# Performance work log

Measured on AMD Instinct MI355X. Metric: run time of the kernel, lower is better.

The kernel has to match this reference:

```python
import jax, jax.numpy as jnp
import numpy as np

B, T, D, U = 64, 4096, 256, 64

def setup_inputs() -> dict:
    key = jax.random.key(0)
    k1, k2, k3 = jax.random.split(key, 3)
    inputs = jax.random.normal(k1, (B, T, D), dtype=jnp.float32)
    # glorot_uniform init for W (D,U) and u (U,1); zeros bias
    limW = float(np.sqrt(6.0 / (D + U)))
    W = jax.random.uniform(k2, (D, U), minval=-limW, maxval=limW, dtype=jnp.float32)
    limu = float(np.sqrt(6.0 / (U + 1)))
    u = jax.random.uniform(k3, (U, 1), minval=-limu, maxval=limu, dtype=jnp.float32)
    b = jnp.zeros((U,), dtype=jnp.float32)
    return {"inputs": inputs, "W": W, "b": b, "u": u}

def reference(inputs, W, b, u):
    # score: [B,T,U] = tanh(inputs @ W + b)
    score = jnp.tanh(jnp.einsum('btd,du->btu', inputs, W) + b)
    # logits: [B,T,1]; softmax over time axis (axis=1)
    logits = jnp.einsum('btu,uo->bto', score, u)
    attention_weights = jax.nn.softmax(logits, axis=1)
    # weighted sum over time -> [B,D]
    context = jnp.sum(inputs * attention_weights, axis=1)
    return (context, attention_weights)
```

## Files before the change

kernel.cpp:

```cpp
#include <hip/hip_runtime.h>
#include <math.h>

#define B_ 64
#define T_ 4096
#define D_ 256
#define U_ 64
#define TM 64
#define ASTRIDE 264
#define TC 256

typedef float f32x4 __attribute__((ext_vector_type(4)));
typedef short bf16x8 __attribute__((ext_vector_type(8)));

__device__ __forceinline__ unsigned short f2bf_rne(float f) {
    unsigned u = __float_as_uint(f);
    unsigned r = u + 0x7fffu + ((u >> 16) & 1u);
    return (unsigned short)(r >> 16);
}
__device__ __forceinline__ float bfbits2f(unsigned short s) {
    return __uint_as_float(((unsigned)s) << 16);
}

__global__ __launch_bounds__(256) void wprep_kernel(
    const float* __restrict__ W, unsigned short* __restrict__ whi,
    unsigned short* __restrict__ wlo)
{
    int fi = blockIdx.x * 256 + threadIdx.x;
    int j    = fi & 7;
    int lane = (fi >> 3) & 63;
    int tile = fi >> 9;
    int nt = tile & 3, ks = tile >> 2;
    int k = ks * 32 + (lane >> 4) * 8 + j;
    int n = nt * 16 + (lane & 15);
    float w = W[k * U_ + n];
    unsigned short hi = f2bf_rne(w);
    unsigned short lo = f2bf_rne(w - bfbits2f(hi));
    whi[fi] = hi;
    wlo[fi] = lo;
}

__global__ __launch_bounds__(256) void logits_mfma(
    const float* __restrict__ x, const unsigned short* __restrict__ whi,
    const unsigned short* __restrict__ wlo, const float* __restrict__ bias,
    const float* __restrict__ uvec, float* __restrict__ logits)
{
    __shared__ unsigned short Ahi[TM * ASTRIDE];
    __shared__ unsigned short Alo[TM * ASTRIDE];

    int tid = threadIdx.x;
    const float4* xb = (const float4*)(x + (size_t)blockIdx.x * TM * D_);

#pragma unroll
    for (int i = 0; i < 16; ++i) {
        int f = tid + i * 256;
        int row = f >> 6, c4 = f & 63;
        float4 v = xb[f];
        unsigned short h0 = f2bf_rne(v.x), h1 = f2bf_rne(v.y),
                       h2 = f2bf_rne(v.z), h3 = f2bf_rne(v.w);
        unsigned short l0 = f2bf_rne(v.x - bfbits2f(h0)),
                       l1 = f2bf_rne(v.y - bfbits2f(h1)),
                       l2 = f2bf_rne(v.z - bfbits2f(h2)),
                       l3 = f2bf_rne(v.w - bfbits2f(h3));
        int base = row * ASTRIDE + c4 * 4;
        uint2 hp = { (unsigned)h0 | ((unsigned)h1 << 16),
                     (unsigned)h2 | ((unsigned)h3 << 16) };
        uint2 lp = { (unsigned)l0 | ((unsigned)l1 << 16),
                     (unsigned)l2 | ((unsigned)l3 << 16) };
        *(uint2*)(&Ahi[base]) = hp;
        *(uint2*)(&Alo[base]) = lp;
    }
    __syncthreads();

    int lane = tid & 63, wid = tid >> 6;
    int q = lane >> 4, r = lane & 15;

    f32x4 acc[4];
#pragma unroll
    for (int nt = 0; nt < 4; ++nt) acc[nt] = (f32x4){0.f, 0.f, 0.f, 0.f};

    const bf16x8* whiV = (const bf16x8*)whi;
    const bf16x8* wloV = (const bf16x8*)wlo;

#pragma unroll
    for (int ks = 0; ks < 8; ++ks) {
        int aoff = (wid * 16 + r) * ASTRIDE + ks * 32 + q * 8;
        bf16x8 ahi = *(const bf16x8*)(&Ahi[aoff]);
        bf16x8 alo = *(const bf16x8*)(&Alo[aoff]);
#pragma unroll
        for (int nt = 0; nt < 4; ++nt) {
            bf16x8 bhi = whiV[(ks * 4 + nt) * 64 + lane];
            bf16x8 blo = wloV[(ks * 4 + nt) * 64 + lane];
            acc[nt] = __builtin_amdgcn_mfma_f32_16x16x32_bf16(ahi, bhi, acc[nt], 0, 0, 0);
            acc[nt] = __builtin_amdgcn_mfma_f32_16x16x32_bf16(ahi, blo, acc[nt], 0, 0, 0);
            acc[nt] = __builtin_amdgcn_mfma_f32_16x16x32_bf16(alo, bhi, acc[nt], 0, 0, 0);
        }
    }

    float p0 = 0.f, p1 = 0.f, p2 = 0.f, p3 = 0.f;
#pragma unroll
    for (int nt = 0; nt < 4; ++nt) {
        int col = nt * 16 + r;
        float bv = bias[col], uv = uvec[col];
        float s0 = acc[nt][0] + bv, s1 = acc[nt][1] + bv,
              s2 = acc[nt][2] + bv, s3 = acc[nt][3] + bv;
        p0 = fmaf(1.f - 2.f / (__expf(2.f * s0) + 1.f), uv, p0);
        p1 = fmaf(1.f - 2.f / (__expf(2.f * s1) + 1.f), uv, p1);
        p2 = fmaf(1.f - 2.f / (__expf(2.f * s2) + 1.f), uv, p2);
        p3 = fmaf(1.f - 2.f / (__expf(2.f * s3) + 1.f), uv, p3);
    }
#pragma unroll
    for (int off = 1; off < 16; off <<= 1) {
        p0 += __shfl_xor(p0, off, 64);
        p1 += __shfl_xor(p1, off, 64);
        p2 += __shfl_xor(p2, off, 64);
        p3 += __shfl_xor(p3, off, 64);
    }
    if (r == 0) {
        float4 o = {p0, p1, p2, p3};
        *(float4*)(logits + (size_t)blockIdx.x * TM + wid * 16 + q * 4) = o;
    }
}

__global__ __launch_bounds__(256) void softmax_kernel(float* __restrict__ wts)
{
    int b = blockIdx.x;
    float* wp = wts + (size_t)b * T_;
    int tid = threadIdx.x;
    int wave = tid >> 6, lane = tid & 63;

    float vals[T_ / 256];
#pragma unroll
    for (int i = 0; i < T_ / 256; ++i) vals[i] = wp[tid + i * 256];

    float m = -INFINITY;
#pragma unroll
    for (int i = 0; i < T_ / 256; ++i) m = fmaxf(m, vals[i]);
#pragma unroll
    for (int off = 32; off >= 1; off >>= 1)
        m = fmaxf(m, __shfl_down(m, off, 64));

    __shared__ float smax[4], ssum[4];
    if (lane == 0) smax[wave] = m;
    __syncthreads();
    if (tid == 0)
        smax[0] = fmaxf(fmaxf(smax[0], smax[1]), fmaxf(smax[2], smax[3]));
    __syncthreads();
    m = smax[0];

    float s = 0.f;
#pragma unroll
    for (int i = 0; i < T_ / 256; ++i) {
        vals[i] = __expf(vals[i] - m);
        s += vals[i];
    }
#pragma unroll
    for (int off = 32; off >= 1; off >>= 1)
        s += __shfl_down(s, off, 64);
    if (lane == 0) ssum[wave] = s;
    __syncthreads();
    if (tid == 0) ssum[0] = ssum[0] + ssum[1] + ssum[2] + ssum[3];
    __syncthreads();

    float inv = 1.f / ssum[0];
#pragma unroll
    for (int i = 0; i < T_ / 256; ++i) wp[tid + i * 256] = vals[i] * inv;
}

__global__ __launch_bounds__(256) void context_kernel(
    const float* __restrict__ x, const float* __restrict__ wts,
    float* __restrict__ ctx)
{
    int b = blockIdx.y;
    int t0 = blockIdx.x * TC;
    int d = threadIdx.x;
    const float* xp = x + ((size_t)b * T_ + t0) * D_ + d;
    const float* wp = wts + (size_t)b * T_ + t0;

    float acc[8];
#pragma unroll
    for (int j = 0; j < 8; ++j) acc[j] = 0.f;

    for (int i = 0; i < TC; i += 8) {
        float w[8], xv[8];
#pragma unroll
        for (int j = 0; j < 8; ++j) w[j] = wp[i + j];
#pragma unroll
        for (int j = 0; j < 8; ++j) xv[j] = xp[(size_t)(i + j) * D_];
#pragma unroll
        for (int j = 0; j < 8; ++j) acc[j] = fmaf(w[j], xv[j], acc[j]);
    }
    float s = ((acc[0] + acc[1]) + (acc[2] + acc[3])) +
              ((acc[4] + acc[5]) + (acc[6] + acc[7]));
    atomicAdd(&ctx[b * D_ + d], s);
}

extern "C" void kernel_launch(void* const* d_in, const int* in_sizes, int n_in,
                              void* d_out, int out_size, void* d_ws, size_t ws_size,
                              hipStream_t stream) {
    const float* x    = (const float*)d_in[0];
    const float* W    = (const float*)d_in[1];
    const float* bias = (const float*)d_in[2];
    const float* uvec = (const float*)d_in[3];

    float* out = (float*)d_out;
    float* ctx = out;
    float* wts = out + B_ * D_;

    unsigned short* whi = (unsigned short*)d_ws;
    unsigned short* wlo = whi + D_ * U_;

    hipMemsetAsync(ctx, 0, B_ * D_ * sizeof(float), stream);

    wprep_kernel<<<D_ * U_ / 256, 256, 0, stream>>>(W, whi, wlo);
    logits_mfma<<<(B_ * T_) / TM, 256, 0, stream>>>(x, whi, wlo, bias, uvec, wts);
    softmax_kernel<<<B_, 256, 0, stream>>>(wts);
    context_kernel<<<dim3(T_ / TC, B_), 256, 0, stream>>>(x, wts, ctx);
}
```

Baseline: 458.0 us.

## Load A fragments directly from global and vectorize context reduction with float4

The logits kernel drops its shared-memory staging of the bf16 hi/lo split. Each lane now loads its 8 floats for every k-step straight from global memory and converts them in registers, which removes about 66KB of LDS and a barrier and so should raise occupancy. The cost is strided per-row global reads instead of fully coalesced ones. The context kernel switches to float4 loads, with four time-slices per block reduced through shared memory before the atomics, which cuts per-thread load count.

```diff
diff --git a/kernel.cpp b/kernel.cpp
--- a/kernel.cpp
+++ b/kernel.cpp
@@ -6,7 +6,6 @@
 #define D_ 256
 #define U_ 64
 #define TM 64
-#define ASTRIDE 264
 #define TC 256
 
 typedef float f32x4 __attribute__((ext_vector_type(4)));
@@ -44,36 +43,13 @@
     const unsigned short* __restrict__ wlo, const float* __restrict__ bias,
     const float* __restrict__ uvec, float* __restrict__ logits)
 {
-    __shared__ unsigned short Ahi[TM * ASTRIDE];
-    __shared__ unsigned short Alo[TM * ASTRIDE];
-
     int tid = threadIdx.x;
-    const float4* xb = (const float4*)(x + (size_t)blockIdx.x * TM * D_);
-
-#pragma unroll
-    for (int i = 0; i < 16; ++i) {
-        int f = tid + i * 256;
-        int row = f >> 6, c4 = f & 63;
-        float4 v = xb[f];
-        unsigned short h0 = f2bf_rne(v.x), h1 = f2bf_rne(v.y),
-                       h2 = f2bf_rne(v.z), h3 = f2bf_rne(v.w);
-        unsigned short l0 = f2bf_rne(v.x - bfbits2f(h0)),
-                       l1 = f2bf_rne(v.y - bfbits2f(h1)),
-                       l2 = f2bf_rne(v.z - bfbits2f(h2)),
-                       l3 = f2bf_rne(v.w - bfbits2f(h3));
-        int base = row * ASTRIDE + c4 * 4;
-        uint2 hp = { (unsigned)h0 | ((unsigned)h1 << 16),
-                     (unsigned)h2 | ((unsigned)h3 << 16) };
-        uint2 lp = { (unsigned)l0 | ((unsigned)l1 << 16),
-                     (unsigned)l2 | ((unsigned)l3 << 16) };
-        *(uint2*)(&Ahi[base]) = hp;
-        *(uint2*)(&Alo[base]) = lp;
-    }
-    __syncthreads();
-
     int lane = tid & 63, wid = tid >> 6;
     int q = lane >> 4, r = lane & 15;
 
+    size_t row = (size_t)blockIdx.x * TM + wid * 16 + r;
+    const float* xrow = x + row * D_;
+
     f32x4 acc[4];
 #pragma unroll
     for (int nt = 0; nt < 4; ++nt) acc[nt] = (f32x4){0.f, 0.f, 0.f, 0.f};
@@ -83,16 +59,24 @@
 
 #pragma unroll
     for (int ks = 0; ks < 8; ++ks) {
-        int aoff = (wid * 16 + r) * ASTRIDE + ks * 32 + q * 8;
-        bf16x8 ahi = *(const bf16x8*)(&Ahi[aoff]);
-        bf16x8 alo = *(const bf16x8*)(&Alo[aoff]);
+        int k0 = ks * 32 + q * 8;
+        float4 va = *(const float4*)(xrow + k0);
+        float4 vb = *(const float4*)(xrow + k0 + 4);
+        float f[8] = {va.x, va.y, va.z, va.w, vb.x, vb.y, vb.z, vb.w};
+        union { bf16x8 v; unsigned short s[8]; } ahi, alo;
+#pragma unroll
+        for (int j = 0; j < 8; ++j) {
+            unsigned short h = f2bf_rne(f[j]);
+            ahi.s[j] = h;
+            alo.s[j] = f2bf_rne(f[j] - bfbits2f(h));
+        }
 #pragma unroll
         for (int nt = 0; nt < 4; ++nt) {
             bf16x8 bhi = whiV[(ks * 4 + nt) * 64 + lane];
             bf16x8 blo = wloV[(ks * 4 + nt) * 64 + lane];
-            acc[nt] = __builtin_amdgcn_mfma_f32_16x16x32_bf16(ahi, bhi, acc[nt], 0, 0, 0);
-            acc[nt] = __builtin_amdgcn_mfma_f32_16x16x32_bf16(ahi, blo, acc[nt], 0, 0, 0);
-            acc[nt] = __builtin_amdgcn_mfma_f32_16x16x32_bf16(alo, bhi, acc[nt], 0, 0, 0);
+            acc[nt] = __builtin_amdgcn_mfma_f32_16x16x32_bf16(ahi.v, bhi, acc[nt], 0, 0, 0);
+            acc[nt] = __builtin_amdgcn_mfma_f32_16x16x32_bf16(ahi.v, blo, acc[nt], 0, 0, 0);
+            acc[nt] = __builtin_amdgcn_mfma_f32_16x16x32_bf16(alo.v, bhi, acc[nt], 0, 0, 0);
         }
     }
 
@@ -172,26 +156,55 @@
 {
     int b = blockIdx.y;
     int t0 = blockIdx.x * TC;
-    int d = threadIdx.x;
-    const float* xp = x + ((size_t)b * T_ + t0) * D_ + d;
-    const float* wp = wts + (size_t)b * T_ + t0;
-
-    float acc[8];
-#pragma unroll
-    for (int j = 0; j < 8; ++j) acc[j] = 0.f;
-
-    for (int i = 0; i < TC; i += 8) {
-        float w[8], xv[8];
-#pragma unroll
-        for (int j = 0; j < 8; ++j) w[j] = wp[i + j];
-#pragma unroll
-        for (int j = 0; j < 8; ++j) xv[j] = xp[(size_t)(i + j) * D_];
-#pragma unroll
-        for (int j = 0; j < 8; ++j) acc[j] = fmaf(w[j], xv[j], acc[j]);
-    }
-    float s = ((acc[0] + acc[1]) + (acc[2] + acc[3])) +
-              ((acc[4] + acc[5]) + (acc[6] + acc[7]));
-    atomicAdd(&ctx[b * D_ + d], s);
+    int tid = threadIdx.x;
+    int d4 = tid & 63;
+    int ts = tid >> 6;
+
+    const float4* xp = (const float4*)(x + ((size_t)b * T_ + t0) * D_) + d4;
+    const float* wp = wts + (size_t)b * T_ + t0 + ts;
+
+    float4 a0 = {0,0,0,0}, a1 = a0, a2 = a0, a3 = a0;
+#pragma unroll 4
+    for (int j = 0; j < TC / 4; j += 4) {
+        float w0 = wp[4 * (j + 0)];
+        float w1 = wp[4 * (j + 1)];
+        float w2 = wp[4 * (j + 2)];
+        float w3 = wp[4 * (j + 3)];
+        float4 x0 = xp[(size_t)(ts + 4 * (j + 0)) * 64];
+        float4 x1 = xp[(size_t)(ts + 4 * (j + 1)) * 64];
+        float4 x2 = xp[(size_t)(ts + 4 * (j + 2)) * 64];
+        float4 x3 = xp[(size_t)(ts + 4 * (j + 3)) * 64];
+        a0.x = fmaf(w0, x0.x, a0.x); a0.y = fmaf(w0, x0.y, a0.y);
+        a0.z = fmaf(w0, x0.z, a0.z); a0.w = fmaf(w0, x0.w, a0.w);
+        a1.x = fmaf(w1, x1.x, a1.x); a1.y = fmaf(w1, x1.y, a1.y);
+        a1.z = fmaf(w1, x1.z, a1.z); a1.w = fmaf(w1, x1.w, a1.w);
+        a2.x = fmaf(w2, x2.x, a2.x); a2.y = fmaf(w2, x2.y, a2.y);
+        a2.z = fmaf(w2, x2.z, a2.z); a2.w = fmaf(w2, x2.w, a2.w);
+        a3.x = fmaf(w3, x3.x, a3.x); a3.y = fmaf(w3, x3.y, a3.y);
+        a3.z = fmaf(w3, x3.z, a3.z); a3.w = fmaf(w3, x3.w, a3.w);
+    }
+    float4 s;
+    s.x = (a0.x + a1.x) + (a2.x + a3.x);
+    s.y = (a0.y + a1.y) + (a2.y + a3.y);
+    s.z = (a0.z + a1.z) + (a2.z + a3.z);
+    s.w = (a0.w + a1.w) + (a2.w + a3.w);
+
+    __shared__ float4 red[4][64];
+    red[ts][d4] = s;
+    __syncthreads();
+    if (ts == 0) {
+        float4 r0 = red[0][d4], r1 = red[1][d4], r2 = red[2][d4], r3 = red[3][d4];
+        float4 t;
+        t.x = (r0.x + r1.x) + (r2.x + r3.x);
+        t.y = (r0.y + r1.y) + (r2.y + r3.y);
+        t.z = (r0.z + r1.z) + (r2.z + r3.z);
+        t.w = (r0.w + r1.w) + (r2.w + r3.w);
+        float* c = ctx + b * D_ + d4 * 4;
+        atomicAdd(c + 0, t.x);
+        atomicAdd(c + 1, t.y);
+        atomicAdd(c + 2, t.z);
+        atomicAdd(c + 3, t.w);
+    }
 }
 
 extern "C" void kernel_launch(void* const* d_in, const int* in_sizes, int n_in,
```

Measured after the change: 424.3 us. -7.4%, faster.

## Fuse softmax into the logits kernel and stream a bf16 copy of x to context

Applied to the files above, without the earlier changes.

The logits kernel now keeps the split-bf16 W in LDS and reads x straight from global memory, with no A-tile staging. It writes exp(logit) with no max subtraction, plus per-block partial sums of the normaliser, so the separate softmax kernel is removed. It also writes a bf16 copy of x, and the context kernel reads that half-size copy to form the weighted sum, normalising by the summed partials. The aim is to cut one launch and the fp32 re-read of x, at the cost of extra writes, lower precision in context, and overflow risk if logits are ever large.

```diff
diff --git a/kernel.cpp b/kernel.cpp
--- a/kernel.cpp
+++ b/kernel.cpp
@@ -5,8 +5,7 @@
 #define T_ 4096
 #define D_ 256
 #define U_ 64
-#define TM 64
-#define ASTRIDE 264
+#define TM 128
 #define TC 256
 
 typedef float f32x4 __attribute__((ext_vector_type(4)));
@@ -42,156 +41,162 @@
 __global__ __launch_bounds__(256) void logits_mfma(
     const float* __restrict__ x, const unsigned short* __restrict__ whi,
     const unsigned short* __restrict__ wlo, const float* __restrict__ bias,
-    const float* __restrict__ uvec, float* __restrict__ logits)
+    const float* __restrict__ uvec, float* __restrict__ wts,
+    unsigned short* __restrict__ xbf, float* __restrict__ Zp)
 {
-    __shared__ unsigned short Ahi[TM * ASTRIDE];
-    __shared__ unsigned short Alo[TM * ASTRIDE];
+    __shared__ unsigned short Bh[16384];
+    __shared__ unsigned short Bl[16384];
+    __shared__ float zred[4];
 
     int tid = threadIdx.x;
-    const float4* xb = (const float4*)(x + (size_t)blockIdx.x * TM * D_);
-
-#pragma unroll
-    for (int i = 0; i < 16; ++i) {
-        int f = tid + i * 256;
-        int row = f >> 6, c4 = f & 63;
-        float4 v = xb[f];
-        unsigned short h0 = f2bf_rne(v.x), h1 = f2bf_rne(v.y),
-                       h2 = f2bf_rne(v.z), h3 = f2bf_rne(v.w);
-        unsigned short l0 = f2bf_rne(v.x - bfbits2f(h0)),
-                       l1 = f2bf_rne(v.y - bfbits2f(h1)),
-                       l2 = f2bf_rne(v.z - bfbits2f(h2)),
-                       l3 = f2bf_rne(v.w - bfbits2f(h3));
-        int base = row * ASTRIDE + c4 * 4;
-        uint2 hp = { (unsigned)h0 | ((unsigned)h1 << 16),
-                     (unsigned)h2 | ((unsigned)h3 << 16) };
-        uint2 lp = { (unsigned)l0 | ((unsigned)l1 << 16),
-                     (unsigned)l2 | ((unsigned)l3 << 16) };
-        *(uint2*)(&Ahi[base]) = hp;
-        *(uint2*)(&Alo[base]) = lp;
+    {
+        const uint4* sh = (const uint4*)whi;
+        const uint4* sl = (const uint4*)wlo;
+        uint4* dh = (uint4*)Bh;
+        uint4* dl = (uint4*)Bl;
+#pragma unroll
+        for (int i = 0; i < 8; ++i) {
+            dh[tid + i * 256] = sh[tid + i * 256];
+            dl[tid + i * 256] = sl[tid + i * 256];
+        }
     }
     __syncthreads();
 
     int lane = tid & 63, wid = tid >> 6;
     int q = lane >> 4, r = lane & 15;
-
-    f32x4 acc[4];
-#pragma unroll
-    for (int nt = 0; nt < 4; ++nt) acc[nt] = (f32x4){0.f, 0.f, 0.f, 0.f};
-
-    const bf16x8* whiV = (const bf16x8*)whi;
-    const bf16x8* wloV = (const bf16x8*)wlo;
-
-#pragma unroll
+    size_t R0 = (size_t)blockIdx.x * TM;
+    size_t row0 = R0 + wid * 16 + r;
+    size_t row1 = row0 + 64;
+    const float* x0 = x + row0 * D_;
+    const float* x1 = x + row1 * D_;
+    unsigned short* xo0 = xbf + row0 * D_;
+    unsigned short* xo1 = xbf + row1 * D_;
+
+    f32x4 acc0[4], acc1[4];
+#pragma unroll
+    for (int nt = 0; nt < 4; ++nt) {
+        acc0[nt] = (f32x4){0.f, 0.f, 0.f, 0.f};
+        acc1[nt] = (f32x4){0.f, 0.f, 0.f, 0.f};
+    }
+
+    const bf16x8* BhV = (const bf16x8*)Bh;
+    const bf16x8* BlV = (const bf16x8*)Bl;
+
+#pragma unroll 4
     for (int ks = 0; ks < 8; ++ks) {
-        int aoff = (wid * 16 + r) * ASTRIDE + ks * 32 + q * 8;
-        bf16x8 ahi = *(const bf16x8*)(&Ahi[aoff]);
-        bf16x8 alo = *(const bf16x8*)(&Alo[aoff]);
+        int k0 = ks * 32 + q * 8;
+        float4 va0 = *(const float4*)(x0 + k0);
+        float4 vb0 = *(const float4*)(x0 + k0 + 4);
+        float4 va1 = *(const float4*)(x1 + k0);
+        float4 vb1 = *(const float4*)(x1 + k0 + 4);
+        float f0[8] = {va0.x, va0.y, va0.z, va0.w, vb0.x, vb0.y, vb0.z, vb0.w};
+        float f1[8] = {va1.x, va1.y, va1.z, va1.w, vb1.x, vb1.y, vb1.z, vb1.w};
+        union { bf16x8 v; unsigned short s[8]; uint4 u; } h0, l0, h1, l1;
+#pragma unroll
+        for (int j = 0; j < 8; ++j) {
+            unsigned short a = f2bf_rne(f0[j]);
+            h0.s[j] = a;
+            l0.s[j] = f2bf_rne(f0[j] - bfbits2f(a));
+            unsigned short c = f2bf_rne(f1[j]);
+            h1.s[j] = c;
+            l1.s[j] = f2bf_rne(f1[j] - bfbits2f(c));
+        }
+        *(uint4*)(xo0 + k0) = h0.u;
+        *(uint4*)(xo1 + k0) = h1.u;
 #pragma unroll
         for (int nt = 0; nt < 4; ++nt) {
-            bf16x8 bhi = whiV[(ks * 4 + nt) * 64 + lane];
-            bf16x8 blo = wloV[(ks * 4 + nt) * 64 + lane];
-            acc[nt] = __builtin_amdgcn_mfma_f32_16x16x32_bf16(ahi, bhi, acc[nt], 0, 0, 0);
-            acc[nt] = __builtin_amdgcn_mfma_f32_16x16x32_bf16(ahi, blo, acc[nt], 0, 0, 0);
-            acc[nt] = __builtin_amdgcn_mfma_f32_16x16x32_bf16(alo, bhi, acc[nt], 0, 0, 0);
-        }
-    }
-
-    float p0 = 0.f, p1 = 0.f, p2 = 0.f, p3 = 0.f;
-#pragma unroll
-    for (int nt = 0; nt < 4; ++nt) {
-        int col = nt * 16 + r;
-        float bv = bias[col], uv = uvec[col];
-        float s0 = acc[nt][0] + bv, s1 = acc[nt][1] + bv,
-              s2 = acc[nt][2] + bv, s3 = acc[nt][3] + bv;
-        p0 = fmaf(1.f - 2.f / (__expf(2.f * s0) + 1.f), uv, p0);
-        p1 = fmaf(1.f - 2.f / (__expf(2.f * s1) + 1.f), uv, p1);
-        p2 = fmaf(1.f - 2.f / (__expf(2.f * s2) + 1.f), uv, p2);
-        p3 = fmaf(1.f - 2.f / (__expf(2.f * s3) + 1.f), uv, p3);
-    }
-#pragma unroll
-    for (int off = 1; off < 16; off <<= 1) {
-        p0 += __shfl_xor(p0, off, 64);
-        p1 += __shfl_xor(p1, off, 64);
-        p2 += __shfl_xor(p2, off, 64);
-        p3 += __shfl_xor(p3, off, 64);
-    }
-    if (r == 0) {
-        float4 o = {p0, p1, p2, p3};
-        *(float4*)(logits + (size_t)blockIdx.x * TM + wid * 16 + q * 4) = o;
-    }
-}
-
-__global__ __launch_bounds__(256) void softmax_kernel(float* __restrict__ wts)
-{
-    int b = blockIdx.x;
-    float* wp = wts + (size_t)b * T_;
-    int tid = threadIdx.x;
-    int wave = tid >> 6, lane = tid & 63;
-
-    float vals[T_ / 256];
-#pragma unroll
-    for (int i = 0; i < T_ / 256; ++i) vals[i] = wp[tid + i * 256];
-
-    float m = -INFINITY;
-#pragma unroll
-    for (int i = 0; i < T_ / 256; ++i) m = fmaxf(m, vals[i]);
-#pragma unroll
-    for (int off = 32; off >= 1; off >>= 1)
-        m = fmaxf(m, __shfl_down(m, off, 64));
-
-    __shared__ float smax[4], ssum[4];
-    if (lane == 0) smax[wave] = m;
-    __syncthreads();
-    if (tid == 0)
-        smax[0] = fmaxf(fmaxf(smax[0], smax[1]), fmaxf(smax[2], smax[3]));
-    __syncthreads();
-    m = smax[0];
-
-    float s = 0.f;
-#pragma unroll
-    for (int i = 0; i < T_ / 256; ++i) {
-        vals[i] = __expf(vals[i] - m);
-        s += vals[i];
-    }
-#pragma unroll
-    for (int off = 32; off >= 1; off >>= 1)
-        s += __shfl_down(s, off, 64);
-    if (lane == 0) ssum[wave] = s;
-    __syncthreads();
-    if (tid == 0) ssum[0] = ssum[0] + ssum[1] + ssum[2] + ssum[3];
-    __syncthreads();
-
-    float inv = 1.f / ssum[0];
-#pragma unroll
-    for (int i = 0; i < T_ / 256; ++i) wp[tid + i * 256] = vals[i] * inv;
+            bf16x8 bh = BhV[(ks * 4 + nt) * 64 + lane];
+            bf16x8 bl = BlV[(ks * 4 + nt) * 64 + lane];
+            acc0[nt] = __builtin_amdgcn_mfma_f32_16x16x32_bf16(h0.v, bh, acc0[nt], 0, 0, 0);
+            acc0[nt] = __builtin_amdgcn_mfma_f32_16x16x32_bf16(h0.v, bl, acc0[nt], 0, 0, 0);
+            acc0[nt] = __builtin_amdgcn_mfma_f32_16x16x32_bf16(l0.v, bh, acc0[nt], 0, 0, 0);
+            acc1[nt] = __builtin_amdgcn_mfma_f32_16x16x32_bf16(h1.v, bh, acc1[nt], 0, 0, 0);
+            acc1[nt] = __builtin_amdgcn_mfma_f32_16x16x32_bf16(h1.v, bl, acc1[nt], 0, 0, 0);
+            acc1[nt] = __builtin_amdgcn_mfma_f32_16x16x32_bf16(l1.v, bh, acc1[nt], 0, 0, 0);
+        }
+    }
+
+    float zsum = 0.f;
+#pragma unroll
+    for (int s = 0; s < 2; ++s) {
+        f32x4* A = s ? acc1 : acc0;
+        float p0 = 0.f, p1 = 0.f, p2 = 0.f, p3 = 0.f;
+#pragma unroll
+        for (int nt = 0; nt < 4; ++nt) {
+            int col = nt * 16 + r;
+            float bv = bias[col], uv = uvec[col];
+            float s0 = A[nt][0] + bv, s1 = A[nt][1] + bv,
+                  s2 = A[nt][2] + bv, s3 = A[nt][3] + bv;
+            p0 = fmaf(1.f - 2.f / (__expf(2.f * s0) + 1.f), uv, p0);
+            p1 = fmaf(1.f - 2.f / (__expf(2.f * s1) + 1.f), uv, p1);
+            p2 = fmaf(1.f - 2.f / (__expf(2.f * s2) + 1.f), uv, p2);
+            p3 = fmaf(1.f - 2.f / (__expf(2.f * s3) + 1.f), uv, p3);
+        }
+#pragma unroll
+        for (int off = 1; off < 16; off <<= 1) {
+            p0 += __shfl_xor(p0, off, 64);
+            p1 += __shfl_xor(p1, off, 64);
+            p2 += __shfl_xor(p2, off, 64);
+            p3 += __shfl_xor(p3, off, 64);
+        }
+        float e0 = __expf(p0), e1 = __expf(p1), e2 = __expf(p2), e3 = __expf(p3);
+        if (r == 0) {
+            float4 o = {e0, e1, e2, e3};
+            *(float4*)(wts + R0 + s * 64 + wid * 16 + q * 4) = o;
+        }
+        zsum += (e0 + e1) + (e2 + e3);
+    }
+    zsum += __shfl_xor(zsum, 16, 64);
+    zsum += __shfl_xor(zsum, 32, 64);
+    if (lane == 0) zred[wid] = zsum;
+    __syncthreads();
+    if (tid == 0) Zp[blockIdx.x] = (zred[0] + zred[1]) + (zred[2] + zred[3]);
 }
 
 __global__ __launch_bounds__(256) void context_kernel(
-    const float* __restrict__ x, const float* __restrict__ wts,
-    float* __restrict__ ctx)
+    const unsigned short* __restrict__ xbf, float* __restrict__ wts,
+    const float* __restrict__ Zp, float* __restrict__ ctx)
 {
     int b = blockIdx.y;
     int t0 = blockIdx.x * TC;
-    int d = threadIdx.x;
-    const float* xp = x + ((size_t)b * T_ + t0) * D_ + d;
-    const float* wp = wts + (size_t)b * T_ + t0;
-
+    int tid = threadIdx.x;
+    int colg = tid & 31, ph = tid >> 5;
+
+    float Z = 0.f;
+#pragma unroll
+    for (int i = 0; i < T_ / TM; ++i) Z += Zp[b * (T_ / TM) + i];
+    float invZ = 1.f / Z;
+
+    __shared__ float wsh[TC];
+    float e = wts[(size_t)b * T_ + t0 + tid];
+    wsh[tid] = e;
+    wts[(size_t)b * T_ + t0 + tid] = e * invZ;
+    __syncthreads();
+
+    const unsigned short* xb = xbf + ((size_t)b * T_ + t0) * D_;
     float acc[8];
 #pragma unroll
     for (int j = 0; j < 8; ++j) acc[j] = 0.f;
 
+#pragma unroll 4
     for (int i = 0; i < TC; i += 8) {
-        float w[8], xv[8];
-#pragma unroll
-        for (int j = 0; j < 8; ++j) w[j] = wp[i + j];
-#pragma unroll
-        for (int j = 0; j < 8; ++j) xv[j] = xp[(size_t)(i + j) * D_];
-#pragma unroll
-        for (int j = 0; j < 8; ++j) acc[j] = fmaf(w[j], xv[j], acc[j]);
-    }
-    float s = ((acc[0] + acc[1]) + (acc[2] + acc[3])) +
-              ((acc[4] + acc[5]) + (acc[6] + acc[7]));
-    atomicAdd(&ctx[b * D_ + d], s);
+        int row = i + ph;
+        float w = wsh[row];
+        union { uint4 u; unsigned short s[8]; } v;
+        v.u = *(const uint4*)(xb + (size_t)row * D_ + colg * 8);
+#pragma unroll
+        for (int j = 0; j < 8; ++j)
+            acc[j] = fmaf(w, bfbits2f(v.s[j]), acc[j]);
+    }
+
+    __shared__ float red[8 * 256];
+#pragma unroll
+    for (int j = 0; j < 8; ++j) red[ph * 256 + colg * 8 + j] = acc[j];
+    __syncthreads();
+    float ssum = 0.f;
+#pragma unroll
+    for (int p = 0; p < 8; ++p) ssum += red[p * 256 + tid];
+    atomicAdd(&ctx[b * D_ + tid], ssum * invZ);
 }
 
 extern "C" void kernel_launch(void* const* d_in, const int* in_sizes, int n_in,
@@ -208,11 +213,12 @@
 
     unsigned short* whi = (unsigned short*)d_ws;
     unsigned short* wlo = whi + D_ * U_;
+    unsigned short* xbf = wlo + D_ * U_;
+    float* Zp = (float*)(xbf + (size_t)B_ * T_ * D_);
 
     hipMemsetAsync(ctx, 0, B_ * D_ * sizeof(float), stream);
 
     wprep_kernel<<<D_ * U_ / 256, 256, 0, stream>>>(W, whi, wlo);
-    logits_mfma<<<(B_ * T_) / TM, 256, 0, stream>>>(x, whi, wlo, bias, uvec, wts);
-    softmax_kernel<<<B_, 256, 0, stream>>>(wts);
-    context_kernel<<<dim3(T_ / TC, B_), 256, 0, stream>>>(x, wts, ctx);
-}
+    logits_mfma<<<(B_ * T_) / TM, 256, 0, stream>>>(x, whi, wlo, bias, uvec, wts, xbf, Zp);
+    context_kernel<<<dim3(T_ / TC, B_), 256, 0, stream>>>(xbf, wts, Zp, ctx);
+}
```

Result: faster. 434.5 us (-5.1%).
